# Kernel optimization log

Hardware: AMD Instinct MI355X
Metric: run time of the kernel (lower is better)

The kernel has to match this reference:

```python
import jax, jax.numpy as jnp
import numpy as np

INPUT_SIZE = 64
HIDDEN = 256
BATCH = 128
SEQ = 1000


def setup_inputs() -> dict:
    key = jax.random.key(0)
    ks = jax.random.split(key, 17)
    s_in = 1.0 / np.sqrt(INPUT_SIZE)
    s_h = 1.0 / np.sqrt(HIDDEN)
    d = {"x": jax.random.normal(ks[0], (BATCH, SEQ, INPUT_SIZE), dtype=jnp.float32)}
    names_ih = ["W_ii", "W_if", "W_ig", "W_io"]
    names_hh = ["W_hi", "W_hf", "W_hg", "W_ho"]
    for i, n in enumerate(names_ih):
        d[n] = jax.random.uniform(ks[1 + i], (HIDDEN, INPUT_SIZE), minval=-s_in, maxval=s_in, dtype=jnp.float32)
        d["b" + n[1:]] = jax.random.uniform(ks[5 + i], (HIDDEN,), minval=-s_in, maxval=s_in, dtype=jnp.float32)
    for i, n in enumerate(names_hh):
        d[n] = jax.random.uniform(ks[9 + i], (HIDDEN, HIDDEN), minval=-s_h, maxval=s_h, dtype=jnp.float32)
        d["b" + n[1:]] = jax.random.uniform(ks[13 + i], (HIDDEN,), minval=-s_h, maxval=s_h, dtype=jnp.float32)
    return d


def _lstm(x, W_ii, b_ii, W_if, b_if, W_ig, b_ig, W_io, b_io,
          W_hi, b_hi, W_hf, b_hf, W_hg, b_hg, W_ho, b_ho):
    B = x.shape[0]
    H = W_ii.shape[0]
    # Precompute all input-to-hidden projections for every timestep in one
    # batched GEMM per gate (the recurrence only needs the h-to-h part).
    # Shapes: [B, T, H] each; then move time to the leading axis for scan.
    xi = jnp.einsum('bti,hi->tbh', x, W_ii) + b_ii
    xf = jnp.einsum('bti,hi->tbh', x, W_if) + b_if
    xg = jnp.einsum('bti,hi->tbh', x, W_ig) + b_ig
    xo = jnp.einsum('bti,hi->tbh', x, W_io) + b_io

    h0 = jnp.zeros((B, H), dtype=x.dtype)
    c0 = jnp.zeros((B, H), dtype=x.dtype)

    def step(carry, xs):
        h, c = carry
        xi_t, xf_t, xg_t, xo_t = xs
        i_t = jax.nn.sigmoid(xi_t + h @ W_hi.T + b_hi)
        f_t = jax.nn.sigmoid(xf_t + h @ W_hf.T + b_hf)
        g_t = jnp.tanh(xg_t + h @ W_hg.T + b_hg)
        o_t = jax.nn.sigmoid(xo_t + h @ W_ho.T + b_ho)
        c_new = f_t * c + i_t * g_t
        h_new = o_t * jnp.tanh(c_new)
        return (h_new, c_new), h_new

    (h_n, c_n), out_tbh = jax.lax.scan(step, (h0, c0), (xi, xf, xg, xo))
    output = jnp.transpose(out_tbh, (1, 0, 2))  # [B, T, H]
    return output, h_n[None], c_n[None]


def reference(x, W_ii, b_ii, W_if, b_if, W_ig, b_ig, W_io, b_io,
              W_hi, b_hi, W_hf, b_hf, W_hg, b_hg, W_ho, b_ho):
    return _lstm(x, W_ii, b_ii, W_if, b_if, W_ig, b_ig, W_io, b_io,
                 W_hi, b_hi, W_hf, b_hf, W_hg, b_hg, W_ho, b_ho)
```

## Files before the change

kernel.cpp:

```cpp
#include <hip/hip_runtime.h>

#define INPUT 64
#define HID 256
#define BATCH 128
#define TSTEPS 1000
#define KTOT 320

typedef __bf16 bf16_t;
typedef __bf16 bf16x8 __attribute__((ext_vector_type(8)));
typedef float  f32x4  __attribute__((ext_vector_type(4)));

#define WPACK_OFF   0
#define WPACK_BYTES (1024 * KTOT * 2)
#define BIAS_OFF    (WPACK_OFF + WPACK_BYTES)
#define BIAS_BYTES  (1024 * 4)
#define EXCH_OFF    (BIAS_OFF + BIAS_BYTES)
#define EXCH_BYTES  (16 * 2 * 2048 * 2)
#define FLAG_OFF    (EXCH_OFF + EXCH_BYTES)

__global__ void lstm_prep(
    const float* __restrict__ Wii, const float* __restrict__ Wif,
    const float* __restrict__ Wig, const float* __restrict__ Wio,
    const float* __restrict__ Whi, const float* __restrict__ Whf,
    const float* __restrict__ Whg, const float* __restrict__ Who,
    const float* __restrict__ bii, const float* __restrict__ bif,
    const float* __restrict__ big, const float* __restrict__ bio,
    const float* __restrict__ bhi, const float* __restrict__ bhf,
    const float* __restrict__ bhg, const float* __restrict__ bho,
    bf16_t* __restrict__ wpack, float* __restrict__ bias,
    int* __restrict__ flags)
{
    int id = blockIdx.x * 256 + threadIdx.x;
    if (id < 1024 * KTOT) {
        int n = id / KTOT, k = id % KTOT;
        int g = n >> 8, j = n & 255;
        const float* Wh = (g == 0) ? Whi : (g == 1) ? Whf : (g == 2) ? Whg : Who;
        const float* Wi = (g == 0) ? Wii : (g == 1) ? Wif : (g == 2) ? Wig : Wio;
        float v = (k < HID) ? Wh[j * HID + k] : Wi[j * INPUT + (k - HID)];
        wpack[id] = (bf16_t)v;
    }
    if (id < 1024) {
        int g = id >> 8, j = id & 255;
        const float* bi = (g == 0) ? bii : (g == 1) ? bif : (g == 2) ? big : bio;
        const float* bh = (g == 0) ? bhi : (g == 1) ? bhf : (g == 2) ? bhg : bho;
        bias[id] = bi[j] + bh[j];
    }
    if (id < 16)
        __hip_atomic_store(flags + id * 64, 0, __ATOMIC_RELAXED, __HIP_MEMORY_SCOPE_AGENT);
}

__device__ __forceinline__ float sigmoid_f(float v) {
    return 1.0f / (1.0f + __expf(-v));
}
__device__ __forceinline__ float tanh_f(float v) {
    return 1.0f - 2.0f / (__expf(2.0f * v) + 1.0f);
}

__global__ __launch_bounds__(512) __attribute__((amdgpu_waves_per_eu(2, 2)))
void lstm_main(
    const float* __restrict__ x, const bf16_t* __restrict__ wpack,
    const float* __restrict__ bias_g, float* __restrict__ out,
    bf16_t* __restrict__ exch, int* __restrict__ flags)
{
    __shared__ __align__(16) bf16_t hxx[2][16 * 328];

    const int bid   = blockIdx.x;
    const int group = bid & 7;
    const int half  = bid >> 3;
    const int tid   = threadIdx.x;
    const int w     = tid >> 6;
    const int l     = tid & 63;
    const int col   = l & 15;
    const int kb    = l >> 4;

    const int jloc  = w * 16 + col;
    const int jglob = half * 128 + jloc;

    bf16x8 bW[4][10];
#pragma unroll
    for (int g = 0; g < 4; ++g) {
        const bf16_t* wrow = wpack + (size_t)(g * 256 + jglob) * KTOT;
#pragma unroll
        for (int ks = 0; ks < 10; ++ks)
            bW[g][ks] = *(const bf16x8*)(wrow + ks * 32 + kb * 8);
    }
#pragma unroll
    for (int g = 0; g < 4; ++g)
#pragma unroll
        for (int ks = 0; ks < 10; ++ks)
            asm volatile("" : "+v"(bW[g][ks]));

    float bias_r[4];
#pragma unroll
    for (int g = 0; g < 4; ++g)
        bias_r[g] = bias_g[g * 256 + jglob];

    float c_st[4] = {0.f, 0.f, 0.f, 0.f};

    const int pbid = (1 - half) * 8 + group;
    int*       flag_me = flags + bid * 64;
    const int* flag_pn = flags + pbid * 64;
    const int  pbase   = (1 - half) * 128;

    const int xb = tid >> 5;
    const int xi = (tid & 31) * 2;
    const float* xbase = x + (size_t)(group * 16 + xb) * (TSTEPS * INPUT) + xi;

    const int prow = tid >> 5;
    const int pe0  = (tid & 31) * 4;

    {
        float2 v = *(const float2*)(xbase);
        hxx[0][xb * 328 + 256 + xi]     = (bf16_t)v.x;
        hxx[0][xb * 328 + 256 + xi + 1] = (bf16_t)v.y;
    }
    float2 xv = *(const float2*)(xbase + INPUT);
    __syncthreads();

#pragma unroll 1
    for (int t = 0; t < TSTEPS; ++t) {
        const int cur = t & 1;
        const int nxt = cur ^ 1;

        if (t + 1 < TSTEPS) {
            hxx[nxt][xb * 328 + 256 + xi]     = (bf16_t)xv.x;
            hxx[nxt][xb * 328 + 256 + xi + 1] = (bf16_t)xv.y;
        }
        if (t + 2 < TSTEPS)
            xv = *(const float2*)(xbase + (size_t)(t + 2) * INPUT);
        if (t > 0) {
            if (l == 0) {
                while (__hip_atomic_load(flag_pn, __ATOMIC_RELAXED, __HIP_MEMORY_SCOPE_AGENT) < t) {}
            }
            const bf16_t* src = exch + ((size_t)pbid * 2 + ((t - 1) & 1)) * 2048
                              + prow * 128 + pe0;
            float2 v;
            asm volatile(
                "global_load_dwordx2 %0, %1, off sc0\n\t"
                "s_waitcnt vmcnt(0)"
                : "=&v"(v) : "v"(src) : "memory");
            *(float2*)&hxx[cur][prow * 328 + pbase + pe0] = v;
        }
        __syncthreads();

        f32x4 acc[4];
#pragma unroll
        for (int g = 0; g < 4; ++g)
            acc[g] = (f32x4){bias_r[g], bias_r[g], bias_r[g], bias_r[g]};

        const bf16_t* arow = &hxx[cur][col * 328 + kb * 8];
        {
            bf16x8 a8 = *(const bf16x8*)(arow + 8 * 32);
            bf16x8 a9 = *(const bf16x8*)(arow + 9 * 32);
#pragma unroll
            for (int g = 0; g < 4; ++g) {
                acc[g] = __builtin_amdgcn_mfma_f32_16x16x32_bf16(a8, bW[g][8], acc[g], 0, 0, 0);
                acc[g] = __builtin_amdgcn_mfma_f32_16x16x32_bf16(a9, bW[g][9], acc[g], 0, 0, 0);
            }
        }
        if (t > 0) {
#pragma unroll
            for (int ks = 0; ks < 8; ++ks) {
                bf16x8 a = *(const bf16x8*)(arow + ks * 32);
#pragma unroll
                for (int g = 0; g < 4; ++g)
                    acc[g] = __builtin_amdgcn_mfma_f32_16x16x32_bf16(a, bW[g][ks], acc[g], 0, 0, 0);
            }
        }

        bf16_t* pub = exch + ((size_t)bid * 2 + cur) * 2048;
        float hv[4];
#pragma unroll
        for (int r = 0; r < 4; ++r) {
            float gi = sigmoid_f(acc[0][r]);
            float gf = sigmoid_f(acc[1][r]);
            float gg = tanh_f(acc[2][r]);
            float go = sigmoid_f(acc[3][r]);
            float c  = gf * c_st[r] + gi * gg;
            c_st[r]  = c;
            float h  = go * tanh_f(c);
            hv[r]    = h;
            bf16_t hb = (bf16_t)h;
            const int row = kb * 4 + r;
            hxx[nxt][row * 328 + jglob] = hb;
            pub[row * 128 + jloc]       = hb;
        }
        __syncthreads();
        if (tid == 0)
            __hip_atomic_store(flag_me, t + 1, __ATOMIC_RELAXED, __HIP_MEMORY_SCOPE_AGENT);

#pragma unroll
        for (int r = 0; r < 4; ++r) {
            const int row = kb * 4 + r;
            const int bg  = group * 16 + row;
            out[((size_t)bg * TSTEPS + t) * HID + jglob] = hv[r];
        }
        if (t == TSTEPS - 1) {
            float* hn = out + (size_t)BATCH * TSTEPS * HID;
            float* cn = hn + (size_t)BATCH * HID;
#pragma unroll
            for (int r = 0; r < 4; ++r) {
                const int row = kb * 4 + r;
                const int bg  = group * 16 + row;
                hn[(size_t)bg * HID + jglob] = hv[r];
                cn[(size_t)bg * HID + jglob] = c_st[r];
            }
        }
    }
}

extern "C" void kernel_launch(void* const* d_in, const int* in_sizes, int n_in,
                              void* d_out, int out_size, void* d_ws, size_t ws_size,
                              hipStream_t stream)
{
    (void)in_sizes; (void)n_in; (void)out_size; (void)ws_size;
    const float* x   = (const float*)d_in[0];
    const float* Wii = (const float*)d_in[1];
    const float* bii = (const float*)d_in[2];
    const float* Wif = (const float*)d_in[3];
    const float* bif = (const float*)d_in[4];
    const float* Wig = (const float*)d_in[5];
    const float* big = (const float*)d_in[6];
    const float* Wio = (const float*)d_in[7];
    const float* bio = (const float*)d_in[8];
    const float* Whi = (const float*)d_in[9];
    const float* bhi = (const float*)d_in[10];
    const float* Whf = (const float*)d_in[11];
    const float* bhf = (const float*)d_in[12];
    const float* Whg = (const float*)d_in[13];
    const float* bhg = (const float*)d_in[14];
    const float* Who = (const float*)d_in[15];
    const float* bho = (const float*)d_in[16];

    char* ws = (char*)d_ws;
    bf16_t* wpack = (bf16_t*)(ws + WPACK_OFF);
    float*  bias  = (float*)(ws + BIAS_OFF);
    bf16_t* exch  = (bf16_t*)(ws + EXCH_OFF);
    int*    flags = (int*)(ws + FLAG_OFF);

    lstm_prep<<<(1024 * KTOT + 255) / 256, 256, 0, stream>>>(
        Wii, Wif, Wig, Wio, Whi, Whf, Whg, Who,
        bii, bif, big, bio, bhi, bhf, bhg, bho,
        wpack, bias, flags);

    lstm_main<<<16, 512, 0, stream>>>(
        x, wpack, bias, (float*)d_out, exch, flags);
}
```

Measured before the change: 2.584 ms.

## Split hidden dimension across four blocks per batch group with all-to-all h exchange

Each batch group of 16 rows is now spread over four 256-thread blocks that each own 64 hidden units, instead of two 512-thread blocks that each own 128. The grid doubles to 32 blocks and each block carries a quarter of the recurrent MFMA work per step. In exchange, every step now needs three partner flags polled and three exchange buffers read instead of one. Exchange stores and loads use sc0 sc1 cache bypass, with an explicit vmcnt wait before the flag release.

```diff
diff --git a/kernel.cpp b/kernel.cpp
--- a/kernel.cpp
+++ b/kernel.cpp
@@ -15,7 +15,7 @@
 #define BIAS_OFF    (WPACK_OFF + WPACK_BYTES)
 #define BIAS_BYTES  (1024 * 4)
 #define EXCH_OFF    (BIAS_OFF + BIAS_BYTES)
-#define EXCH_BYTES  (16 * 2 * 2048 * 2)
+#define EXCH_BYTES  (32 * 2 * 1024 * 2)
 #define FLAG_OFF    (EXCH_OFF + EXCH_BYTES)
 
 __global__ void lstm_prep(
@@ -45,7 +45,7 @@
         const float* bh = (g == 0) ? bhi : (g == 1) ? bhf : (g == 2) ? bhg : bho;
         bias[id] = bi[j] + bh[j];
     }
-    if (id < 16)
+    if (id < 32)
         __hip_atomic_store(flags + id * 64, 0, __ATOMIC_RELAXED, __HIP_MEMORY_SCOPE_AGENT);
 }
 
@@ -56,7 +56,7 @@
     return 1.0f - 2.0f / (__expf(2.0f * v) + 1.0f);
 }
 
-__global__ __launch_bounds__(512) __attribute__((amdgpu_waves_per_eu(2, 2)))
+__global__ __launch_bounds__(256) __attribute__((amdgpu_waves_per_eu(1, 1)))
 void lstm_main(
     const float* __restrict__ x, const bf16_t* __restrict__ wpack,
     const float* __restrict__ bias_g, float* __restrict__ out,
@@ -66,15 +66,15 @@
 
     const int bid   = blockIdx.x;
     const int group = bid & 7;
-    const int half  = bid >> 3;
+    const int qtr   = bid >> 3;
     const int tid   = threadIdx.x;
     const int w     = tid >> 6;
     const int l     = tid & 63;
     const int col   = l & 15;
     const int kb    = l >> 4;
 
-    const int jloc  = w * 16 + col;
-    const int jglob = half * 128 + jloc;
+    const int jblk  = w * 16 + col;
+    const int jglob = qtr * 64 + jblk;
 
     bf16x8 bW[4][10];
 #pragma unroll
@@ -97,24 +97,25 @@
 
     float c_st[4] = {0.f, 0.f, 0.f, 0.f};
 
-    const int pbid = (1 - half) * 8 + group;
-    int*       flag_me = flags + bid * 64;
+    int* flag_me = flags + bid * 64;
+    const int p      = tid >> 6;
+    const int pi     = tid & 63;
+    const int pqtr   = (qtr + 1 + p) & 3;
+    const int pbid   = pqtr * 8 + group;
     const int* flag_pn = flags + pbid * 64;
-    const int  pbase   = (1 - half) * 128;
-
-    const int xb = tid >> 5;
-    const int xi = (tid & 31) * 2;
-    const float* xbase = x + (size_t)(group * 16 + xb) * (TSTEPS * INPUT) + xi;
-
-    const int prow = tid >> 5;
-    const int pe0  = (tid & 31) * 4;
+    const int prow   = pi >> 2;
+    const int pc16   = (pi & 3) * 16;
+
+    const int xr  = tid >> 4;
+    const int xi0 = (tid & 15) * 4;
+    const float* xbase = x + (size_t)(group * 16 + xr) * (TSTEPS * INPUT) + xi0;
 
     {
-        float2 v = *(const float2*)(xbase);
-        hxx[0][xb * 328 + 256 + xi]     = (bf16_t)v.x;
-        hxx[0][xb * 328 + 256 + xi + 1] = (bf16_t)v.y;
-    }
-    float2 xv = *(const float2*)(xbase + INPUT);
+        float4 v = *(const float4*)(xbase);
+        bf16_t* d = &hxx[0][xr * 328 + 256 + xi0];
+        d[0] = (bf16_t)v.x; d[1] = (bf16_t)v.y; d[2] = (bf16_t)v.z; d[3] = (bf16_t)v.w;
+    }
+    float4 xv = *(const float4*)(xbase + INPUT);
     __syncthreads();
 
 #pragma unroll 1
@@ -123,23 +124,26 @@
         const int nxt = cur ^ 1;
 
         if (t + 1 < TSTEPS) {
-            hxx[nxt][xb * 328 + 256 + xi]     = (bf16_t)xv.x;
-            hxx[nxt][xb * 328 + 256 + xi + 1] = (bf16_t)xv.y;
+            bf16_t* d = &hxx[nxt][xr * 328 + 256 + xi0];
+            d[0] = (bf16_t)xv.x; d[1] = (bf16_t)xv.y; d[2] = (bf16_t)xv.z; d[3] = (bf16_t)xv.w;
         }
         if (t + 2 < TSTEPS)
-            xv = *(const float2*)(xbase + (size_t)(t + 2) * INPUT);
-        if (t > 0) {
-            if (l == 0) {
-                while (__hip_atomic_load(flag_pn, __ATOMIC_RELAXED, __HIP_MEMORY_SCOPE_AGENT) < t) {}
-            }
-            const bf16_t* src = exch + ((size_t)pbid * 2 + ((t - 1) & 1)) * 2048
-                              + prow * 128 + pe0;
-            float2 v;
+            xv = *(const float4*)(xbase + (size_t)(t + 2) * INPUT);
+        if (t > 0 && w < 3) {
+            while (__hip_atomic_load(flag_pn, __ATOMIC_RELAXED, __HIP_MEMORY_SCOPE_AGENT) < t) {}
+            const bf16_t* src = exch + ((size_t)pbid * 2 + ((t - 1) & 1)) * 1024
+                              + prow * 64 + pc16;
+            f32x4 v0, v1;
             asm volatile(
-                "global_load_dwordx2 %0, %1, off sc0\n\t"
+                "global_load_dwordx4 %0, %2, off sc0 sc1\n\t"
+                "global_load_dwordx4 %1, %3, off sc0 sc1\n\t"
                 "s_waitcnt vmcnt(0)"
-                : "=&v"(v) : "v"(src) : "memory");
-            *(float2*)&hxx[cur][prow * 328 + pbase + pe0] = v;
+                : "=&v"(v0), "=&v"(v1)
+                : "v"(src), "v"(src + 8)
+                : "memory");
+            bf16_t* dst = &hxx[cur][prow * 328 + pqtr * 64 + pc16];
+            *(f32x4*)(dst)     = v0;
+            *(f32x4*)(dst + 8) = v1;
         }
         __syncthreads();
 
@@ -168,7 +172,7 @@
             }
         }
 
-        bf16_t* pub = exch + ((size_t)bid * 2 + cur) * 2048;
+        bf16_t* pub = exch + ((size_t)bid * 2 + cur) * 1024;
         float hv[4];
 #pragma unroll
         for (int r = 0; r < 4; ++r) {
@@ -183,8 +187,12 @@
             bf16_t hb = (bf16_t)h;
             const int row = kb * 4 + r;
             hxx[nxt][row * 328 + jglob] = hb;
-            pub[row * 128 + jloc]       = hb;
-        }
+            unsigned int hbits = (unsigned int)__builtin_bit_cast(unsigned short, hb);
+            const bf16_t* paddr = pub + row * 64 + jblk;
+            asm volatile("global_store_short %0, %1, off sc0 sc1"
+                         :: "v"(paddr), "v"(hbits) : "memory");
+        }
+        asm volatile("s_waitcnt vmcnt(0)" ::: "memory");
         __syncthreads();
         if (tid == 0)
             __hip_atomic_store(flag_me, t + 1, __ATOMIC_RELAXED, __HIP_MEMORY_SCOPE_AGENT);
@@ -243,6 +251,6 @@
         bii, bif, big, bio, bhi, bhf, bhg, bho,
         wpack, bias, flags);
 
-    lstm_main<<<16, 512, 0, stream>>>(
+    lstm_main<<<32, 256, 0, stream>>>(
         x, wpack, bias, (float*)d_out, exch, flags);
 }
```

Result: faster. 2.419 ms (-6.4%).
